# Optimization experiments

Hardware: AMD Instinct MI355X
Metric: run time of the kernel (lower is better)

## Reference

```python
import jax, jax.numpy as jnp
import numpy as np

EMBED = 512
INPUT = 512
NEGINF = -1000000.0


def setup_inputs() -> dict:
    key = jax.random.key(0)
    k1, k2, k3, k4, k5, k6, k7 = jax.random.split(key, 7)
    B, S = 8, 2048
    return {
        "Xin_q": jax.random.normal(k1, (B, S, INPUT), dtype=jnp.float32),
        "Xin_k": jax.random.normal(k2, (B, S, INPUT), dtype=jnp.float32),
        "Xin_v": jax.random.normal(k3, (B, S, INPUT), dtype=jnp.float32),
        "mask": jax.random.randint(k4, (B, S, S), 0, 2, dtype=jnp.int32),
        # Linear weights stored as (input, embed) so projection is x @ W
        "Wq": jax.random.normal(k5, (INPUT, EMBED), dtype=jnp.float32) / np.sqrt(INPUT),
        "Wk": jax.random.normal(k6, (INPUT, EMBED), dtype=jnp.float32) / np.sqrt(INPUT),
        "Wv": jax.random.normal(k7, (INPUT, EMBED), dtype=jnp.float32) / np.sqrt(INPUT),
    }


def reference(Xin_q, Xin_k, Xin_v, mask, Wq, Wk, Wv):
    scale = EMBED ** 0.25  # each of Q and K divided by d^(1/4) -> QK^T / sqrt(d)
    Xq = (Xin_q @ Wq) / scale          # [B,S,E]
    Xk = (Xin_k @ Wk) / scale          # [B,S,E]
    Xv = Xin_v @ Wv                    # [B,S,E]
    attn_w = jnp.einsum("bqe,bke->bqk", Xq, Xk)  # [B,S,S]
    attn_w = jnp.where(mask == 0, NEGINF, attn_w)
    attn_p = jax.nn.softmax(attn_w, axis=2)
    # post-softmax unnormalized mask-multiply (nonstandard)
    attn_p = attn_p * mask.astype(attn_p.dtype)
    z = jnp.einsum("bqk,bke->bqe", attn_p, Xv)   # [B,S,E]
    return (z, attn_p)
```

## Files before the change

### kernel.cpp

```cpp
#include <hip/hip_runtime.h>
#include <stdint.h>

typedef __attribute__((ext_vector_type(8))) short short8;
typedef __attribute__((ext_vector_type(4))) float f32x4;
typedef __attribute__((ext_vector_type(4))) int i32x4;
typedef __attribute__((ext_vector_type(8))) unsigned short ushort8v;

#define NEGINF_F (-1000000.0f)

__device__ __forceinline__ unsigned short f2bf(float f) {
  union { float f; uint32_t u; } v; v.f = f;
  uint32_t r = (v.u + 0x7FFFu + ((v.u >> 16) & 1u)) >> 16;
  return (unsigned short)r;
}
__device__ __forceinline__ void gl_lds16(const void* g, void* l) {
  __builtin_amdgcn_global_load_lds(
      (const __attribute__((address_space(1))) void*)g,
      (__attribute__((address_space(3))) void*)l, 16, 0, 0);
}

template<bool A32, bool OUT32, bool MASKED>
__global__ __launch_bounds__(256, A32 ? 2 : 4)
void gemm_nt(const void* __restrict__ Av, const unsigned short* __restrict__ B,
             void* __restrict__ Cv, const int* __restrict__ mask,
             int K, int lda, int ldb, int ldc,
             long sA, long sB, long sC, long sM, float scale)
{
  constexpr int ABYTES = A32 ? 128 * 32 * 4 : 128 * 32 * 2;
  constexpr int BBYTES = 128 * 32 * 2;
  constexpr int BUFB = ABYTES + BBYTES;
  __shared__ __align__(16) unsigned char smem[2 * BUFB];

  const int t = threadIdx.x;
  const int b = blockIdx.z;
  const float* Af = (const float*)Av + (long)b * sA;
  const unsigned short* Ah = (const unsigned short*)Av + (long)b * sA;
  const unsigned short* Bp = B + (long)b * sB;
  const int* mp = MASKED ? (mask + (long)b * sM) : nullptr;
  const int tm = blockIdx.x * 128;
  const int tn = blockIdx.y * 128;

  const int lane = t & 63, wave = t >> 6;
  const int wm = (wave & 1) * 64, wn = (wave >> 1) * 64;
  const int q = lane >> 4, mr = lane & 15;

  f32x4 acc[4][4];
#pragma unroll
  for (int i = 0; i < 4; i++)
#pragma unroll
    for (int j = 0; j < 4; j++) acc[i][j] = (f32x4){0.f, 0.f, 0.f, 0.f};

  const int r0a = t >> 2;
  const int cswz = ((t & 3) ^ ((t >> 2) & 3)) * 8;
  const int sw8 = (q ^ (mr & 3)) * 8;

  auto stage = [&](int buf, int k0) {
    unsigned char* base = smem + buf * BUFB;
    if (A32) {
      float* Asf = (float*)base;
#pragma unroll
      for (int rd = 0; rd < 4; rd++) {
        const int f = rd * 1024 + t * 4;
        const int row = f >> 5, col = f & 31;
        gl_lds16(Af + (long)(tm + row) * lda + k0 + col, Asf + f);
      }
    } else {
      unsigned short* Ash = (unsigned short*)base;
      const unsigned short* ga = Ah + (long)(tm + r0a) * lda + k0 + cswz;
      gl_lds16(ga, &Ash[(size_t)t * 8]);
      gl_lds16(ga + (long)64 * lda, &Ash[(size_t)(t + 256) * 8]);
    }
    unsigned short* Bsb = (unsigned short*)(base + ABYTES);
    const unsigned short* gb = Bp + (long)(tn + r0a) * ldb + k0 + cswz;
    gl_lds16(gb, &Bsb[(size_t)t * 8]);
    gl_lds16(gb + (long)64 * ldb, &Bsb[(size_t)(t + 256) * 8]);
  };

  const int nt = K >> 5;
  stage(0, 0);
  __syncthreads();

  for (int ti = 0; ti < nt; ++ti) {
    if (ti + 1 < nt) stage((ti + 1) & 1, (ti + 1) << 5);

    const unsigned char* base = smem + (ti & 1) * BUFB;
    const unsigned short* Bs = (const unsigned short*)(base + ABYTES);
    short8 af[4], bfr[4];
#pragma unroll
    for (int i = 0; i < 4; i++) {
      if (A32) {
        const float* Asf = (const float*)base;
        const int fb = (wm + i * 16 + mr) * 32 + q * 8;
        const f32x4 x0 = *(const f32x4*)&Asf[fb];
        const f32x4 x1 = *(const f32x4*)&Asf[fb + 4];
        short8 v;
        v[0] = (short)f2bf(x0[0]); v[1] = (short)f2bf(x0[1]);
        v[2] = (short)f2bf(x0[2]); v[3] = (short)f2bf(x0[3]);
        v[4] = (short)f2bf(x1[0]); v[5] = (short)f2bf(x1[1]);
        v[6] = (short)f2bf(x1[2]); v[7] = (short)f2bf(x1[3]);
        af[i] = v;
      } else {
        const unsigned short* Ash = (const unsigned short*)base;
        af[i] = *(const short8*)&Ash[(size_t)(wm + i * 16 + mr) * 32 + sw8];
      }
      bfr[i] = *(const short8*)&Bs[(size_t)(wn + i * 16 + mr) * 32 + sw8];
    }
#pragma unroll
    for (int i = 0; i < 4; i++)
#pragma unroll
      for (int j = 0; j < 4; j++)
        acc[i][j] = __builtin_amdgcn_mfma_f32_16x16x32_bf16(
            af[i], bfr[j], acc[i][j], 0, 0, 0);

    if (ti + 1 < nt) __syncthreads();
  }

  if (OUT32) {
    float* ep = (float*)smem;
    float* co = (float*)Cv + (long)b * sC;
    const int band = wm >> 2;
    const int tr = t >> 3;
    const int tcb = (t & 7) * 16;
    const int growb = tm + (tr >> 4) * 64 + (tr & 15);
#pragma unroll
    for (int i = 0; i < 4; i++) {
      __syncthreads();
#pragma unroll
      for (int j = 0; j < 4; j++) {
        const int colb = wn + j * 16 + mr;
#pragma unroll
        for (int r = 0; r < 4; r++) {
          const int lr = band + q * 4 + r;
          ep[lr * 128 + ((colb + lr * 4) & 127)] = acc[i][j][r];
        }
      }
      __syncthreads();
      const int gr = growb + i * 16;
      const long rbase = (long)gr * ldc;
      const float* eprow = ep + tr * 128;
      const int rot = tr * 4;
#pragma unroll
      for (int k = 0; k < 4; k++) {
        const int lc = tcb + k * 4;
        f32x4 x = *(const f32x4*)&eprow[(lc + rot) & 127];
        x *= scale;
        if (MASKED) {
          const i32x4 mv = *(const i32x4*)&mp[rbase + tn + lc];
#pragma unroll
          for (int e = 0; e < 4; e++)
            if (!mv[e]) x[e] = NEGINF_F;
        }
        *(f32x4*)&co[rbase + tn + lc] = x;
      }
    }
  } else {
#pragma unroll
    for (int i = 0; i < 4; i++) {
#pragma unroll
      for (int j = 0; j < 4; j++) {
        const int row0 = tm + wm + i * 16 + q * 4;
        const int col  = tn + wn + j * 16 + mr;
        const f32x4 v = acc[i][j];
#pragma unroll
        for (int r = 0; r < 4; r++) {
          float x = v[r] * scale;
          ((unsigned short*)Cv + (long)b * sC)[(long)(row0 + r) * ldc + col] = f2bf(x);
        }
      }
    }
  }
}

__global__ __launch_bounds__(256) void softmax_rows_f32(
    float* __restrict__ P, unsigned short* __restrict__ Pb)
{
  const int row = blockIdx.x;
  float* p = P + (size_t)row * 2048;
  const int t = threadIdx.x, lane = t & 63, wv = t >> 6;
  f32x4 a = *(const f32x4*)(p + t * 8);
  f32x4 c = *(const f32x4*)(p + t * 8 + 4);
  float x[8] = {a[0], a[1], a[2], a[3], c[0], c[1], c[2], c[3]};
  float mx = x[0];
#pragma unroll
  for (int j = 1; j < 8; j++) mx = fmaxf(mx, x[j]);
#pragma unroll
  for (int o = 32; o > 0; o >>= 1) mx = fmaxf(mx, __shfl_xor(mx, o));
  __shared__ float rm[4], rs[4];
  if (lane == 0) rm[wv] = mx;
  __syncthreads();
  mx = fmaxf(fmaxf(rm[0], rm[1]), fmaxf(rm[2], rm[3]));
  float e[8], s = 0.f;
#pragma unroll
  for (int j = 0; j < 8; j++) { e[j] = __expf(x[j] - mx); s += e[j]; }
#pragma unroll
  for (int o = 32; o > 0; o >>= 1) s += __shfl_xor(s, o);
  if (lane == 0) rs[wv] = s;
  __syncthreads();
  s = rs[0] + rs[1] + rs[2] + rs[3];
  const float linv = (mx < -1.0e5f) ? 0.f : 1.f / s;
  f32x4 o0 = {e[0] * linv, e[1] * linv, e[2] * linv, e[3] * linv};
  f32x4 o1 = {e[4] * linv, e[5] * linv, e[6] * linv, e[7] * linv};
  *(f32x4*)(p + t * 8) = o0;
  *(f32x4*)(p + t * 8 + 4) = o1;
  if (Pb) {
    ushort8v ob;
    ob[0] = f2bf(o0[0]); ob[1] = f2bf(o0[1]); ob[2] = f2bf(o0[2]); ob[3] = f2bf(o0[3]);
    ob[4] = f2bf(o1[0]); ob[5] = f2bf(o1[1]); ob[6] = f2bf(o1[2]); ob[7] = f2bf(o1[3]);
    *(ushort8v*)(Pb + (size_t)row * 2048 + t * 8) = ob;
  }
}

__global__ __launch_bounds__(256) void cvt2(
    const float* __restrict__ s0, unsigned short* __restrict__ d0,
    const float* __restrict__ s1, unsigned short* __restrict__ d1)
{
  const float* s = blockIdx.y ? s1 : s0;
  unsigned short* d = blockIdx.y ? d1 : d0;
  const size_t i = ((size_t)blockIdx.x * 256 + threadIdx.x) * 8;
  const float4 a = *(const float4*)(s + i);
  const float4 b = *(const float4*)(s + i + 4);
  ushort8v o;
  o[0] = f2bf(a.x); o[1] = f2bf(a.y); o[2] = f2bf(a.z); o[3] = f2bf(a.w);
  o[4] = f2bf(b.x); o[5] = f2bf(b.y); o[6] = f2bf(b.z); o[7] = f2bf(b.w);
  *(ushort8v*)(d + i) = o;
}

__global__ __launch_bounds__(256) void cvt_t_v(
    const float* __restrict__ src, unsigned short* __restrict__ dst)
{
  const int b = blockIdx.z;
  __shared__ float tile[32][33];
  const int s0 = blockIdx.x * 32, i0 = blockIdx.y * 32;
  const int tx = threadIdx.x & 31, ty = threadIdx.x >> 5;
#pragma unroll
  for (int r = 0; r < 4; r++) {
    const int srow = ty + r * 8;
    tile[srow][tx] = src[((size_t)b * 2048 + s0 + srow) * 512 + i0 + tx];
  }
  __syncthreads();
#pragma unroll
  for (int r = 0; r < 4; r++) {
    const int irow = ty + r * 8;
    dst[((size_t)b * 512 + i0 + irow) * 2048 + s0 + tx] = f2bf(tile[tx][irow]);
  }
}

__global__ __launch_bounds__(256) void transpose_w(
    const float* __restrict__ W0, const float* __restrict__ W1,
    const float* __restrict__ W2,
    unsigned short* __restrict__ T0, unsigned short* __restrict__ T1,
    unsigned short* __restrict__ T2)
{
  const float* W = blockIdx.z == 0 ? W0 : (blockIdx.z == 1 ? W1 : W2);
  unsigned short* T = blockIdx.z == 0 ? T0 : (blockIdx.z == 1 ? T1 : T2);
  __shared__ float tile[32][33];
  const int bx = blockIdx.x * 32, by = blockIdx.y * 32;
  const int tx = threadIdx.x & 31, ty = threadIdx.x >> 5;
#pragma unroll
  for (int i = 0; i < 4; i++) {
    const int r = ty + i * 8;
    tile[r][tx] = W[(size_t)(by + r) * 512 + bx + tx];
  }
  __syncthreads();
#pragma unroll
  for (int i = 0; i < 4; i++) {
    const int r = ty + i * 8;
    T[(size_t)(bx + r) * 512 + by + tx] = f2bf(tile[tx][r]);
  }
}

extern "C" void kernel_launch(void* const* d_in, const int* in_sizes, int n_in,
                              void* d_out, int out_size, void* d_ws, size_t ws_size,
                              hipStream_t stream) {
  const float* Xq = (const float*)d_in[0];
  const float* Xk = (const float*)d_in[1];
  const float* Xv = (const float*)d_in[2];
  const int*   mk = (const int*)d_in[3];
  const float* Wq = (const float*)d_in[4];
  const float* Wk = (const float*)d_in[5];
  const float* Wv = (const float*)d_in[6];

  float* z = (float*)d_out;
  float* P = z + (size_t)8 * 2048 * 512;

  unsigned short* w    = (unsigned short*)d_ws;
  unsigned short* Wtq  = w;
  unsigned short* Wtk  = w + 262144;
  unsigned short* Wtv  = w + 524288;
  unsigned short* buf1 = w + 786432;
  unsigned short* buf2 = buf1 + 8388608;
  unsigned short* Ks   = buf2 + 8388608;
  unsigned short* Pb   = Ks;
  const bool use_pb = ws_size >= (size_t)102236160;

  unsigned short* Xkb = (unsigned short*)P;

  const float inv_scale = 0.21022410381342863f;

  transpose_w<<<dim3(16, 16, 3), 256, 0, stream>>>(Wq, Wk, Wv, Wtq, Wtk, Wtv);

  cvt2<<<dim3(4096, 2), 256, 0, stream>>>(Xq, buf1, Xk, Xkb);

  gemm_nt<false, false, false><<<dim3(128, 4, 1), 256, 0, stream>>>(
      buf1, Wtq, buf2, nullptr, 512, 512, 512, 512, 0, 0, 0, 0, inv_scale);

  gemm_nt<false, false, false><<<dim3(128, 4, 1), 256, 0, stream>>>(
      Xkb, Wtk, Ks, nullptr, 512, 512, 512, 512, 0, 0, 0, 0, inv_scale);

  gemm_nt<false, true, true><<<dim3(16, 16, 8), 256, 0, stream>>>(
      buf2, Ks, P, mk, 512, 512, 512, 2048,
      1048576, 1048576, 4194304, 4194304, 1.0f);

  softmax_rows_f32<<<dim3(16384), 256, 0, stream>>>(P, use_pb ? Pb : nullptr);

  cvt_t_v<<<dim3(64, 16, 8), 256, 0, stream>>>(Xv, buf1);
  if (use_pb) {
    gemm_nt<false, false, false><<<dim3(16, 4, 8), 256, 0, stream>>>(
        Pb, buf1, buf2, nullptr, 2048, 2048, 2048, 512,
        4194304, 1048576, 1048576, 0, 1.0f);
  } else {
    gemm_nt<true, false, false><<<dim3(16, 4, 8), 256, 0, stream>>>(
        P, buf1, buf2, nullptr, 2048, 2048, 2048, 512,
        4194304, 1048576, 1048576, 0, 1.0f);
  }
  gemm_nt<false, true, false><<<dim3(128, 4, 1), 256, 0, stream>>>(
      buf2, Wtv, z, nullptr, 512, 512, 512, 512, 0, 0, 0, 0, 1.0f);
}
```

Measured before the change: 519.1 us.

## Add 256x256 tiled QK^T GEMM and reorder V projection before PV

Replaces the QK^T masked GEMM with a new 512-thread kernel using 256x256 tiles, a 4-stage global_load_lds pipeline with explicit vmcnt waits and MFMA priority hints. It also converts Xv to bf16 in the same conversion kernel and computes V^T projection (Wv^T·Xv^T) first, so the PV GEMM writes z directly, dropping the transpose kernel and the final projection GEMM. The larger tile raises register and LDS pressure and runs one block per CU. The mask epilogue now reads the mask with scalar loads per element.

```diff
diff --git a/kernel.cpp b/kernel.cpp
--- a/kernel.cpp
+++ b/kernel.cpp
@@ -7,6 +7,7 @@
 typedef __attribute__((ext_vector_type(8))) unsigned short ushort8v;
 
 #define NEGINF_F (-1000000.0f)
+#define MFMA16 __builtin_amdgcn_mfma_f32_16x16x32_bf16
 
 __device__ __forceinline__ unsigned short f2bf(float f) {
   union { float f; uint32_t u; } v; v.f = f;
@@ -17,6 +18,110 @@
   __builtin_amdgcn_global_load_lds(
       (const __attribute__((address_space(1))) void*)g,
       (__attribute__((address_space(3))) void*)l, 16, 0, 0);
+}
+#define BARRIER() asm volatile("s_barrier" ::: "memory")
+
+__global__ __launch_bounds__(512, 1)
+void gemm256(const unsigned short* __restrict__ A,
+             const unsigned short* __restrict__ B,
+             float* __restrict__ C, const int* __restrict__ mask,
+             int K, int lda, int ldb, int ldc,
+             long sA, long sB, long sC, long sM)
+{
+  __shared__ __align__(16) unsigned short lds[65536];
+
+  const int t = threadIdx.x;
+  const int b = blockIdx.z;
+  const unsigned short* Ap = A + (long)b * sA;
+  const unsigned short* Bp = B + (long)b * sB;
+  const int* mp = mask + (long)b * sM;
+  const int tm = blockIdx.x * 256;
+  const int tn = blockIdx.y * 256;
+
+  const int lane = t & 63, wave = t >> 6;
+  const int wm = (wave >> 2) * 128;
+  const int wn = (wave & 3) * 64;
+  const int q = lane >> 4, mr = lane & 15;
+
+  f32x4 acc[8][4];
+#pragma unroll
+  for (int m = 0; m < 8; m++)
+#pragma unroll
+    for (int n = 0; n < 4; n++) acc[m][n] = (f32x4){0.f, 0.f, 0.f, 0.f};
+
+  const int srow = t >> 2;
+  const int scol = (t & 3) * 8;
+
+  auto stage = [&](int kt) {
+    unsigned short* L = lds + (kt & 3) * 16384;
+    const int k0 = kt << 5;
+    const unsigned short* ga = Ap + (long)(tm + srow) * lda + k0 + scol;
+    gl_lds16(ga,                  L + (size_t)t * 8);
+    gl_lds16(ga + (long)128 * lda, L + 4096 + (size_t)t * 8);
+    const unsigned short* gb = Bp + (long)(tn + srow) * ldb + k0 + scol;
+    gl_lds16(gb,                  L + 8192 + (size_t)t * 8);
+    gl_lds16(gb + (long)128 * ldb, L + 12288 + (size_t)t * 8);
+  };
+
+  auto compute = [&](int kt) {
+    const unsigned short* LA = lds + (kt & 3) * 16384;
+    const unsigned short* LB = LA + 8192;
+    short8 af[8], b0, b1;
+#pragma unroll
+    for (int m = 0; m < 8; m++)
+      af[m] = *(const short8*)&LA[(size_t)(wm + m * 16 + mr) * 32 + q * 8];
+    b0 = *(const short8*)&LB[(size_t)(wn + 0 * 16 + mr) * 32 + q * 8];
+    b1 = *(const short8*)&LB[(size_t)(wn + 1 * 16 + mr) * 32 + q * 8];
+    __builtin_amdgcn_s_setprio(1);
+#pragma unroll
+    for (int m = 0; m < 8; m++) acc[m][0] = MFMA16(af[m], b0, acc[m][0], 0, 0, 0);
+#pragma unroll
+    for (int m = 0; m < 8; m++) acc[m][1] = MFMA16(af[m], b1, acc[m][1], 0, 0, 0);
+    __builtin_amdgcn_s_setprio(0);
+    BARRIER();
+    b0 = *(const short8*)&LB[(size_t)(wn + 2 * 16 + mr) * 32 + q * 8];
+    b1 = *(const short8*)&LB[(size_t)(wn + 3 * 16 + mr) * 32 + q * 8];
+    __builtin_amdgcn_s_setprio(1);
+#pragma unroll
+    for (int m = 0; m < 8; m++) acc[m][2] = MFMA16(af[m], b0, acc[m][2], 0, 0, 0);
+#pragma unroll
+    for (int m = 0; m < 8; m++) acc[m][3] = MFMA16(af[m], b1, acc[m][3], 0, 0, 0);
+    __builtin_amdgcn_s_setprio(0);
+  };
+
+  const int NT = K >> 5;
+  stage(0); stage(1); stage(2);
+
+  for (int kt = 0; kt < NT - 3; ++kt) {
+    stage(kt + 3);
+    asm volatile("s_waitcnt vmcnt(12)" ::: "memory");
+    BARRIER();
+    compute(kt);
+    BARRIER();
+  }
+  asm volatile("s_waitcnt vmcnt(8)" ::: "memory");
+  BARRIER(); compute(NT - 3); BARRIER();
+  asm volatile("s_waitcnt vmcnt(4)" ::: "memory");
+  BARRIER(); compute(NT - 2); BARRIER();
+  asm volatile("s_waitcnt vmcnt(0)" ::: "memory");
+  BARRIER(); compute(NT - 1);
+
+  float* co = C + (long)b * sC;
+#pragma unroll
+  for (int m = 0; m < 8; m++) {
+#pragma unroll
+    for (int n = 0; n < 4; n++) {
+      const int row0 = tm + wm + m * 16 + q * 4;
+      const int col  = tn + wn + n * 16 + mr;
+#pragma unroll
+      for (int r = 0; r < 4; r++) {
+        float x = acc[m][n][r];
+        const long idx = (long)(row0 + r) * ldc + col;
+        if (!mp[idx]) x = NEGINF_F;
+        co[idx] = x;
+      }
+    }
+  }
 }
 
 template<bool A32, bool OUT32, bool MASKED>
@@ -109,8 +214,7 @@
     for (int i = 0; i < 4; i++)
 #pragma unroll
       for (int j = 0; j < 4; j++)
-        acc[i][j] = __builtin_amdgcn_mfma_f32_16x16x32_bf16(
-            af[i], bfr[j], acc[i][j], 0, 0, 0);
+        acc[i][j] = MFMA16(af[i], bfr[j], acc[i][j], 0, 0, 0);
 
     if (ti + 1 < nt) __syncthreads();
   }
@@ -210,12 +314,13 @@
   }
 }
 
-__global__ __launch_bounds__(256) void cvt2(
+__global__ __launch_bounds__(256) void cvt3(
     const float* __restrict__ s0, unsigned short* __restrict__ d0,
-    const float* __restrict__ s1, unsigned short* __restrict__ d1)
-{
-  const float* s = blockIdx.y ? s1 : s0;
-  unsigned short* d = blockIdx.y ? d1 : d0;
+    const float* __restrict__ s1, unsigned short* __restrict__ d1,
+    const float* __restrict__ s2, unsigned short* __restrict__ d2)
+{
+  const float* s = blockIdx.y == 0 ? s0 : (blockIdx.y == 1 ? s1 : s2);
+  unsigned short* d = blockIdx.y == 0 ? d0 : (blockIdx.y == 1 ? d1 : d2);
   const size_t i = ((size_t)blockIdx.x * 256 + threadIdx.x) * 8;
   const float4 a = *(const float4*)(s + i);
   const float4 b = *(const float4*)(s + i + 4);
@@ -294,12 +399,13 @@
   const bool use_pb = ws_size >= (size_t)102236160;
 
   unsigned short* Xkb = (unsigned short*)P;
+  unsigned short* Xvb = (unsigned short*)z;
 
   const float inv_scale = 0.21022410381342863f;
 
   transpose_w<<<dim3(16, 16, 3), 256, 0, stream>>>(Wq, Wk, Wv, Wtq, Wtk, Wtv);
 
-  cvt2<<<dim3(4096, 2), 256, 0, stream>>>(Xq, buf1, Xk, Xkb);
+  cvt3<<<dim3(4096, 3), 256, 0, stream>>>(Xq, buf1, Xk, Xkb, Xv, Xvb);
 
   gemm_nt<false, false, false><<<dim3(128, 4, 1), 256, 0, stream>>>(
       buf1, Wtq, buf2, nullptr, 512, 512, 512, 512, 0, 0, 0, 0, inv_scale);
@@ -307,22 +413,25 @@
   gemm_nt<false, false, false><<<dim3(128, 4, 1), 256, 0, stream>>>(
       Xkb, Wtk, Ks, nullptr, 512, 512, 512, 512, 0, 0, 0, 0, inv_scale);
 
-  gemm_nt<false, true, true><<<dim3(16, 16, 8), 256, 0, stream>>>(
+  gemm256<<<dim3(8, 8, 8), 512, 0, stream>>>(
       buf2, Ks, P, mk, 512, 512, 512, 2048,
-      1048576, 1048576, 4194304, 4194304, 1.0f);
+      1048576, 1048576, 4194304, 4194304);
 
   softmax_rows_f32<<<dim3(16384), 256, 0, stream>>>(P, use_pb ? Pb : nullptr);
 
-  cvt_t_v<<<dim3(64, 16, 8), 256, 0, stream>>>(Xv, buf1);
   if (use_pb) {
-    gemm_nt<false, false, false><<<dim3(16, 4, 8), 256, 0, stream>>>(
-        Pb, buf1, buf2, nullptr, 2048, 2048, 2048, 512,
+    gemm_nt<false, false, false><<<dim3(4, 16, 8), 256, 0, stream>>>(
+        Wtv, Xvb, buf2, nullptr, 512, 512, 512, 2048,
+        0, 1048576, 1048576, 0, 1.0f);
+    gemm_nt<false, true, false><<<dim3(16, 4, 8), 256, 0, stream>>>(
+        Pb, buf2, z, nullptr, 2048, 2048, 2048, 512,
         4194304, 1048576, 1048576, 0, 1.0f);
   } else {
+    cvt_t_v<<<dim3(64, 16, 8), 256, 0, stream>>>(Xv, buf1);
     gemm_nt<true, false, false><<<dim3(16, 4, 8), 256, 0, stream>>>(
         P, buf1, buf2, nullptr, 2048, 2048, 2048, 512,
         4194304, 1048576, 1048576, 0, 1.0f);
-  }
-  gemm_nt<false, true, false><<<dim3(128, 4, 1), 256, 0, stream>>>(
-      buf2, Wtv, z, nullptr, 512, 512, 512, 512, 0, 0, 0, 0, 1.0f);
-}
+    gemm_nt<false, true, false><<<dim3(128, 4, 1), 256, 0, stream>>>(
+        buf2, Wtv, z, nullptr, 512, 512, 512, 512, 0, 0, 0, 0, 1.0f);
+  }
+}
```

After: 523.6 us. Within noise of the previous version (+0.9%).

## Batch Q/K projections, move masking into softmax, project V before PV

Applied to the files above, without the earlier changes.

Q and K projections now run as one batched GEMM launch, with a single cvt3 kernel converting all three inputs to bf16. The mask is applied inside the softmax kernel instead of in the QK^T epilogue. On the bf16-P path, V is projected first so the PV GEMM writes z directly in fp32, which removes the transpose kernel and the final projection GEMM. This cuts launches and intermediate traffic, at the cost of reading the mask in the softmax pass and using z as scratch space.

```diff
diff --git a/kernel.cpp b/kernel.cpp
--- a/kernel.cpp
+++ b/kernel.cpp
@@ -7,6 +7,7 @@
 typedef __attribute__((ext_vector_type(8))) unsigned short ushort8v;
 
 #define NEGINF_F (-1000000.0f)
+#define MFMA16 __builtin_amdgcn_mfma_f32_16x16x32_bf16
 
 __device__ __forceinline__ unsigned short f2bf(float f) {
   union { float f; uint32_t u; } v; v.f = f;
@@ -19,12 +20,12 @@
       (__attribute__((address_space(3))) void*)l, 16, 0, 0);
 }
 
-template<bool A32, bool OUT32, bool MASKED>
+template<bool A32, bool OUT32>
 __global__ __launch_bounds__(256, A32 ? 2 : 4)
 void gemm_nt(const void* __restrict__ Av, const unsigned short* __restrict__ B,
-             void* __restrict__ Cv, const int* __restrict__ mask,
+             void* __restrict__ Cv,
              int K, int lda, int ldb, int ldc,
-             long sA, long sB, long sC, long sM, float scale)
+             long sA, long sB, long sC, float scale)
 {
   constexpr int ABYTES = A32 ? 128 * 32 * 4 : 128 * 32 * 2;
   constexpr int BBYTES = 128 * 32 * 2;
@@ -36,7 +37,6 @@
   const float* Af = (const float*)Av + (long)b * sA;
   const unsigned short* Ah = (const unsigned short*)Av + (long)b * sA;
   const unsigned short* Bp = B + (long)b * sB;
-  const int* mp = MASKED ? (mask + (long)b * sM) : nullptr;
   const int tm = blockIdx.x * 128;
   const int tn = blockIdx.y * 128;
 
@@ -109,8 +109,7 @@
     for (int i = 0; i < 4; i++)
 #pragma unroll
       for (int j = 0; j < 4; j++)
-        acc[i][j] = __builtin_amdgcn_mfma_f32_16x16x32_bf16(
-            af[i], bfr[j], acc[i][j], 0, 0, 0);
+        acc[i][j] = MFMA16(af[i], bfr[j], acc[i][j], 0, 0, 0);
 
     if (ti + 1 < nt) __syncthreads();
   }
@@ -144,12 +143,6 @@
         const int lc = tcb + k * 4;
         f32x4 x = *(const f32x4*)&eprow[(lc + rot) & 127];
         x *= scale;
-        if (MASKED) {
-          const i32x4 mv = *(const i32x4*)&mp[rbase + tn + lc];
-#pragma unroll
-          for (int e = 0; e < 4; e++)
-            if (!mv[e]) x[e] = NEGINF_F;
-        }
         *(f32x4*)&co[rbase + tn + lc] = x;
       }
     }
@@ -171,15 +164,24 @@
   }
 }
 
-__global__ __launch_bounds__(256) void softmax_rows_f32(
-    float* __restrict__ P, unsigned short* __restrict__ Pb)
-{
-  const int row = blockIdx.x;
-  float* p = P + (size_t)row * 2048;
+__global__ __launch_bounds__(256) void softmax_mask(
+    float* __restrict__ P, const int* __restrict__ mk,
+    unsigned short* __restrict__ Pb)
+{
+  const size_t row = blockIdx.x;
+  float* p = P + row * 2048;
+  const int* m = mk + row * 2048;
   const int t = threadIdx.x, lane = t & 63, wv = t >> 6;
   f32x4 a = *(const f32x4*)(p + t * 8);
   f32x4 c = *(const f32x4*)(p + t * 8 + 4);
-  float x[8] = {a[0], a[1], a[2], a[3], c[0], c[1], c[2], c[3]};
+  const i32x4 ma = *(const i32x4*)(m + t * 8);
+  const i32x4 mc = *(const i32x4*)(m + t * 8 + 4);
+  float x[8];
+#pragma unroll
+  for (int j = 0; j < 4; j++) {
+    x[j]     = ma[j] ? a[j] : NEGINF_F;
+    x[j + 4] = mc[j] ? c[j] : NEGINF_F;
+  }
   float mx = x[0];
 #pragma unroll
   for (int j = 1; j < 8; j++) mx = fmaxf(mx, x[j]);
@@ -206,16 +208,17 @@
     ushort8v ob;
     ob[0] = f2bf(o0[0]); ob[1] = f2bf(o0[1]); ob[2] = f2bf(o0[2]); ob[3] = f2bf(o0[3]);
     ob[4] = f2bf(o1[0]); ob[5] = f2bf(o1[1]); ob[6] = f2bf(o1[2]); ob[7] = f2bf(o1[3]);
-    *(ushort8v*)(Pb + (size_t)row * 2048 + t * 8) = ob;
-  }
-}
-
-__global__ __launch_bounds__(256) void cvt2(
+    *(ushort8v*)(Pb + row * 2048 + t * 8) = ob;
+  }
+}
+
+__global__ __launch_bounds__(256) void cvt3(
     const float* __restrict__ s0, unsigned short* __restrict__ d0,
-    const float* __restrict__ s1, unsigned short* __restrict__ d1)
-{
-  const float* s = blockIdx.y ? s1 : s0;
-  unsigned short* d = blockIdx.y ? d1 : d0;
+    const float* __restrict__ s1, unsigned short* __restrict__ d1,
+    const float* __restrict__ s2, unsigned short* __restrict__ d2)
+{
+  const float* s = blockIdx.y == 0 ? s0 : (blockIdx.y == 1 ? s1 : s2);
+  unsigned short* d = blockIdx.y == 0 ? d0 : (blockIdx.y == 1 ? d1 : d2);
   const size_t i = ((size_t)blockIdx.x * 256 + threadIdx.x) * 8;
   const float4 a = *(const float4*)(s + i);
   const float4 b = *(const float4*)(s + i + 4);
@@ -285,44 +288,44 @@
 
   unsigned short* w    = (unsigned short*)d_ws;
   unsigned short* Wtq  = w;
-  unsigned short* Wtk  = w + 262144;
   unsigned short* Wtv  = w + 524288;
   unsigned short* buf1 = w + 786432;
   unsigned short* buf2 = buf1 + 8388608;
-  unsigned short* Ks   = buf2 + 8388608;
-  unsigned short* Pb   = Ks;
+  unsigned short* Pb   = buf2 + 8388608;
   const bool use_pb = ws_size >= (size_t)102236160;
 
-  unsigned short* Xkb = (unsigned short*)P;
+  unsigned short* Xqkb = (unsigned short*)P;
+  unsigned short* Xvb  = (unsigned short*)z;
 
   const float inv_scale = 0.21022410381342863f;
 
-  transpose_w<<<dim3(16, 16, 3), 256, 0, stream>>>(Wq, Wk, Wv, Wtq, Wtk, Wtv);
-
-  cvt2<<<dim3(4096, 2), 256, 0, stream>>>(Xq, buf1, Xk, Xkb);
-
-  gemm_nt<false, false, false><<<dim3(128, 4, 1), 256, 0, stream>>>(
-      buf1, Wtq, buf2, nullptr, 512, 512, 512, 512, 0, 0, 0, 0, inv_scale);
-
-  gemm_nt<false, false, false><<<dim3(128, 4, 1), 256, 0, stream>>>(
-      Xkb, Wtk, Ks, nullptr, 512, 512, 512, 512, 0, 0, 0, 0, inv_scale);
-
-  gemm_nt<false, true, true><<<dim3(16, 16, 8), 256, 0, stream>>>(
-      buf2, Ks, P, mk, 512, 512, 512, 2048,
-      1048576, 1048576, 4194304, 4194304, 1.0f);
-
-  softmax_rows_f32<<<dim3(16384), 256, 0, stream>>>(P, use_pb ? Pb : nullptr);
-
-  cvt_t_v<<<dim3(64, 16, 8), 256, 0, stream>>>(Xv, buf1);
+  transpose_w<<<dim3(16, 16, 3), 256, 0, stream>>>(Wq, Wk, Wv, Wtq, Wtq + 262144, Wtv);
+
+  cvt3<<<dim3(4096, 3), 256, 0, stream>>>(Xq, Xqkb, Xk, Xqkb + 8388608, Xv, Xvb);
+
+  gemm_nt<false, false><<<dim3(128, 4, 2), 256, 0, stream>>>(
+      Xqkb, Wtq, buf1, 512, 512, 512, 512,
+      8388608, 262144, 8388608, inv_scale);
+
+  gemm_nt<false, true><<<dim3(16, 16, 8), 256, 0, stream>>>(
+      buf1, buf2, P, 512, 512, 512, 2048,
+      1048576, 1048576, 4194304, 1.0f);
+
+  softmax_mask<<<dim3(16384), 256, 0, stream>>>(P, mk, use_pb ? Pb : nullptr);
+
   if (use_pb) {
-    gemm_nt<false, false, false><<<dim3(16, 4, 8), 256, 0, stream>>>(
-        Pb, buf1, buf2, nullptr, 2048, 2048, 2048, 512,
-        4194304, 1048576, 1048576, 0, 1.0f);
+    gemm_nt<false, false><<<dim3(4, 16, 8), 256, 0, stream>>>(
+        Wtv, Xvb, buf1, 512, 512, 512, 2048,
+        0, 1048576, 1048576, 1.0f);
+    gemm_nt<false, true><<<dim3(16, 4, 8), 256, 0, stream>>>(
+        Pb, buf1, z, 2048, 2048, 2048, 512,
+        4194304, 1048576, 1048576, 1.0f);
   } else {
-    gemm_nt<true, false, false><<<dim3(16, 4, 8), 256, 0, stream>>>(
-        P, buf1, buf2, nullptr, 2048, 2048, 2048, 512,
-        4194304, 1048576, 1048576, 0, 1.0f);
-  }
-  gemm_nt<false, true, false><<<dim3(128, 4, 1), 256, 0, stream>>>(
-      buf2, Wtv, z, nullptr, 512, 512, 512, 512, 0, 0, 0, 0, 1.0f);
-}
+    cvt_t_v<<<dim3(64, 16, 8), 256, 0, stream>>>(Xv, (unsigned short*)buf1);
+    gemm_nt<true, false><<<dim3(16, 4, 8), 256, 0, stream>>>(
+        P, buf1, buf2, 2048, 2048, 2048, 512,
+        4194304, 1048576, 1048576, 1.0f);
+    gemm_nt<false, true><<<dim3(128, 4, 1), 256, 0, stream>>>(
+        buf2, Wtv, z, 512, 512, 512, 512, 0, 0, 0, 1.0f);
+  }
+}
```

Result: slower. 530.2 us (+2.1%).
